# Optimization experiments

Measured on AMD Instinct MI355X. Metric: run time of the kernel, lower is better.

The kernel has to match this reference:

```python
import math
import jax, jax.numpy as jnp
import numpy as np

jax.config.update("jax_enable_x64", True)

# ---- module hyperparameters (init_kwargs) ----
BS, NDIM, NSTEP, ORDER = 16, 16, 128, 2
NIV, NIVSTEPS = 2, 1
P = ORDER + 1                 # number of derivative channels u^(0)..u^(order)
N = NSTEP * P                 # unknowns per system
FACT = np.array([math.factorial(k) for k in range(P)], dtype=np.float64)

# Hard initial-value constraint matrix C (same sparsity for every system)
_C = np.zeros((NIVSTEPS * NIV, N), dtype=np.float64)
for _t in range(NIVSTEPS):
    for _i in range(NIV):
        _C[_t * NIV + _i, _t * P + _i] = 1.0
C = jnp.asarray(_C)
NC = C.shape[0]


def setup_inputs() -> dict:
    key = jax.random.key(0)
    k1, k2, k3, k4 = jax.random.split(key, 4)
    coeffs = jax.random.normal(k1, (BS, NDIM, NSTEP, P), dtype=jnp.float32)
    rhs = jax.random.normal(k2, (BS, NDIM, NSTEP), dtype=jnp.float32)
    iv_rhs = jax.random.normal(k3, (BS, NDIM, NIVSTEPS, NIV), dtype=jnp.float32)
    # step sizes must be positive; keep them in [0.1, 0.2] for good conditioning
    steps = 0.1 + 0.1 * jax.random.uniform(k4, (BS, NDIM, NSTEP - 1), dtype=jnp.float32)
    return {"coeffs": coeffs, "rhs": rhs, "iv_rhs": iv_rhs, "steps": steps}


def _build_A(coeffs, h):
    """Soft-constraint matrix for one scalar ODE system.
    coeffs: (NSTEP, P) f64   ODE coefficients per step
    h:      (NSTEP-1,) f64   step sizes
    Rows: [equation | fwd/bwd Taylor smoothness per order | top-order diff].
    Smoothness rows are normalized by the local truncation error h^(order+1-i).
    """
    n = NSTEP
    t = jnp.arange(n - 1)
    # equation constraints: sum_i c[t,i] u[t,i] = rhs[t]
    A_eq = jnp.zeros((n, N)).at[jnp.repeat(jnp.arange(n), P), jnp.arange(N)].set(coeffs.ravel())
    blocks = [A_eq]
    for i in range(ORDER):
        scale = h ** (-(ORDER + 1 - i))          # (n-1,)
        Af = jnp.zeros((n - 1, N))
        Ab = jnp.zeros((n - 1, N))
        for j in range(i, P):
            cf = (h ** (j - i)) / FACT[j - i]
            cb = ((-h) ** (j - i)) / FACT[j - i]
            Af = Af.at[t, t * P + j].set(scale * cf)        # forward Taylor from step t
            Ab = Ab.at[t, (t + 1) * P + j].set(scale * cb)  # backward Taylor from step t+1
        Af = Af.at[t, (t + 1) * P + i].set(-scale)
        Ab = Ab.at[t, t * P + i].set(-scale)
        blocks += [Af, Ab]
    # highest derivative varies slowly: (u[t+1,K] - u[t,K]) / h ~ 0
    Atop = (jnp.zeros((n - 1, N))
            .at[t, (t + 1) * P + ORDER].set(1.0 / h)
            .at[t, t * P + ORDER].set(-1.0 / h))
    blocks.append(Atop)
    return jnp.concatenate(blocks, axis=0)   # (m, N), m = n + 2(n-1)K + (n-1)


def _solve_one(coeffs, rhs, iv, h):
    """min ||A u - b||^2  s.t.  C u = iv  (KKT solve), one system."""
    A = _build_A(coeffs, h)
    m = A.shape[0]
    b = jnp.concatenate([rhs, jnp.zeros(m - NSTEP)])
    G = A.T @ A                                  # (N, N) banded normal matrix
    Atb = A.T @ b
    M = jnp.block([[G, C.T], [C, jnp.zeros((NC, NC))]])
    v = jnp.concatenate([Atb, iv.ravel()])
    x = jnp.linalg.solve(M, v)
    return x[:N].reshape(NSTEP, P)


def reference(coeffs, rhs, iv_rhs, steps):
    coeffs64 = coeffs.reshape(BS, NDIM, NSTEP, P).astype(jnp.float64)
    rhs64 = rhs.reshape(BS, NDIM, NSTEP).astype(jnp.float64)
    iv64 = iv_rhs.reshape(BS, NDIM, NIVSTEPS, NIV).astype(jnp.float64)
    h64 = steps.reshape(BS, NDIM, NSTEP - 1).astype(jnp.float64)
    solve = jax.vmap(jax.vmap(_solve_one))
    u = solve(coeffs64, rhs64, iv64, h64)        # (BS, NDIM, NSTEP, P)
    u0, u1, u2 = u[..., 0], u[..., 1], u[..., 2]
    return (u0, u1, u2, jnp.zeros(()), h64.reshape(BS * NDIM, NSTEP - 1, 1))
```

## Files before the change

### kernel.cpp

```cpp
#include <hip/hip_runtime.h>
#include <math.h>

#define NSTEP_ 128
#define NSYS_  256
#define STRIDE 21

__device__ __forceinline__ void sym_inv3(const double D[9], double Dinv[9]) {
    const double a = D[0], b = D[3], c = D[4], d = D[6], e = D[7], f = D[8];
    const double A00 = c*f - e*e;
    const double A01 = d*e - b*f;
    const double A02 = b*e - c*d;
    const double A11 = a*f - d*d;
    const double A12 = b*d - a*e;
    const double A22 = a*c - b*b;
    const double det  = a*A00 + b*A01 + d*A02;
    const double idet = 1.0 / det;
    Dinv[0] = A00*idet; Dinv[1] = A01*idet; Dinv[2] = A02*idet;
    Dinv[3] = A01*idet; Dinv[4] = A11*idet; Dinv[5] = A12*idet;
    Dinv[6] = A02*idet; Dinv[7] = A12*idet; Dinv[8] = A22*idet;
}

__device__ __forceinline__ void iface_rows(double h, double wL[5][3], double wR[5][3]) {
    const double ih = 1.0 / h;
    const double s1 = ih * ih;
    const double s0 = s1 * ih;
    const double hh = 0.5 * ih;
    wL[0][0] =  s0; wL[0][1] =  s1; wL[0][2] =  hh;
    wR[0][0] = -s0; wR[0][1] = 0.0; wR[0][2] = 0.0;
    wL[1][0] = -s0; wL[1][1] = 0.0; wL[1][2] = 0.0;
    wR[1][0] =  s0; wR[1][1] = -s1; wR[1][2] =  hh;
    wL[2][0] = 0.0; wL[2][1] =  s1; wL[2][2] =  ih;
    wR[2][0] = 0.0; wR[2][1] = -s1; wR[2][2] = 0.0;
    wL[3][0] = 0.0; wL[3][1] = -s1; wL[3][2] = 0.0;
    wR[3][0] = 0.0; wR[3][1] =  s1; wR[3][2] = -ih;
    wL[4][0] = 0.0; wL[4][1] = 0.0; wL[4][2] = -ih;
    wR[4][0] = 0.0; wR[4][1] = 0.0; wR[4][2] =  ih;
}

__global__ __launch_bounds__(128)
void ode_pcr_solve(const float* __restrict__ coeffs,
                   const float* __restrict__ rhs,
                   const float* __restrict__ ivr,
                   const float* __restrict__ steps,
                   float* __restrict__ out)
{
    const int sys = blockIdx.x;
    const int t   = threadIdx.x;

    const float* cP  = coeffs + (size_t)sys * NSTEP_ * 3;
    const float* rP  = rhs    + (size_t)sys * NSTEP_;
    const float* ivP = ivr    + (size_t)sys * 2;
    const float* hP  = steps  + (size_t)sys * (NSTEP_ - 1);

    __shared__ double sh[NSTEP_ * STRIDE];

    double D[9], U[9], r[3];
    {
        const double cv0 = (double)cP[t*3+0];
        const double cv1 = (double)cP[t*3+1];
        const double cv2 = (double)cP[t*3+2];
        const double rv  = (double)rP[t];
        const double cv[3] = {cv0, cv1, cv2};
        #pragma unroll
        for (int a = 0; a < 3; ++a) {
            #pragma unroll
            for (int b = 0; b < 3; ++b) { D[a*3+b] = cv[a]*cv[b]; U[a*3+b] = 0.0; }
            r[a] = cv[a]*rv;
        }
        if (t < NSTEP_-1) {
            double wL[5][3], wR[5][3];
            iface_rows((double)hP[t], wL, wR);
            #pragma unroll
            for (int k = 0; k < 5; ++k)
                #pragma unroll
                for (int a = 0; a < 3; ++a)
                    #pragma unroll
                    for (int b = 0; b < 3; ++b) {
                        D[a*3+b] += wL[k][a]*wL[k][b];
                        U[a*3+b] += wL[k][a]*wR[k][b];
                    }
        }
        if (t >= 1) {
            double wL[5][3], wR[5][3];
            iface_rows((double)hP[t-1], wL, wR);
            #pragma unroll
            for (int k = 0; k < 5; ++k)
                #pragma unroll
                for (int a = 0; a < 3; ++a)
                    #pragma unroll
                    for (int b = 0; b < 3; ++b)
                        D[a*3+b] += wR[k][a]*wR[k][b];
            if (t == 1) {
                const double iv0 = (double)ivP[0];
                const double iv1 = (double)ivP[1];
                #pragma unroll
                for (int b = 0; b < 3; ++b) {
                    double u0b = 0.0, u1b = 0.0;
                    #pragma unroll
                    for (int k = 0; k < 5; ++k) {
                        u0b += wL[k][0]*wR[k][b];
                        u1b += wL[k][1]*wR[k][b];
                    }
                    r[b] -= u0b*iv0 + u1b*iv1;
                }
            }
        }
        if (t == 0) {
            const double iv0 = (double)ivP[0];
            const double iv1 = (double)ivP[1];
            r[2] -= D[2*3+0]*iv0 + D[2*3+1]*iv1;
            r[0] = iv0; r[1] = iv1;
            #pragma unroll
            for (int a = 0; a < 3; ++a) { D[0*3+a]=0.0; D[1*3+a]=0.0; D[a*3+0]=0.0; D[a*3+1]=0.0; }
            D[0] = 1.0; D[4] = 1.0;
            #pragma unroll
            for (int b = 0; b < 3; ++b) { U[0*3+b] = 0.0; U[1*3+b] = 0.0; }
        }
    }

    #pragma unroll 1
    for (int d = 1; d < NSTEP_; d <<= 1) {
        double Dinv[9];
        sym_inv3(D, Dinv);
        double* row = &sh[t * STRIDE];
        #pragma unroll
        for (int i = 0; i < 9; ++i) row[i]      = Dinv[i];
        #pragma unroll
        for (int i = 0; i < 9; ++i) row[9 + i]  = U[i];
        #pragma unroll
        for (int i = 0; i < 3; ++i) row[18 + i] = r[i];
        __syncthreads();

        double nD[9], nU[9], nr[3];
        #pragma unroll
        for (int i = 0; i < 9; ++i) { nD[i] = D[i]; nU[i] = 0.0; }
        #pragma unroll
        for (int i = 0; i < 3; ++i) nr[i] = r[i];

        if (t + d < NSTEP_) {
            const double* rp_ = &sh[(t + d) * STRIDE];
            double Tp[9];
            #pragma unroll
            for (int a = 0; a < 3; ++a)
                #pragma unroll
                for (int l = 0; l < 3; ++l) {
                    double s = 0.0;
                    #pragma unroll
                    for (int k = 0; k < 3; ++k) s += U[a*3+k] * rp_[k*3+l];
                    Tp[a*3+l] = s;
                }
            #pragma unroll
            for (int a = 0; a < 3; ++a) {
                #pragma unroll
                for (int b = 0; b < 3; ++b) {
                    double su = 0.0, sd = 0.0;
                    #pragma unroll
                    for (int l = 0; l < 3; ++l) {
                        su += Tp[a*3+l] * rp_[9 + l*3+b];
                        sd += Tp[a*3+l] * U[b*3+l];
                    }
                    nU[a*3+b] = -su;
                    nD[a*3+b] -= sd;
                }
                double sr = 0.0;
                #pragma unroll
                for (int l = 0; l < 3; ++l) sr += Tp[a*3+l] * rp_[18 + l];
                nr[a] -= sr;
            }
        }
        if (t - d >= 0) {
            const double* rm_ = &sh[(t - d) * STRIDE];
            double Tm[9];
            #pragma unroll
            for (int a = 0; a < 3; ++a)
                #pragma unroll
                for (int l = 0; l < 3; ++l) {
                    double s = 0.0;
                    #pragma unroll
                    for (int k = 0; k < 3; ++k) s += rm_[9 + k*3+a] * rm_[k*3+l];
                    Tm[a*3+l] = s;
                }
            #pragma unroll
            for (int a = 0; a < 3; ++a) {
                #pragma unroll
                for (int b = 0; b < 3; ++b) {
                    double sd = 0.0;
                    #pragma unroll
                    for (int l = 0; l < 3; ++l) sd += Tm[a*3+l] * rm_[9 + l*3+b];
                    nD[a*3+b] -= sd;
                }
                double sr = 0.0;
                #pragma unroll
                for (int l = 0; l < 3; ++l) sr += Tm[a*3+l] * rm_[18 + l];
                nr[a] -= sr;
            }
        }
        __syncthreads();
        #pragma unroll
        for (int i = 0; i < 9; ++i) { D[i] = nD[i]; U[i] = nU[i]; }
        #pragma unroll
        for (int i = 0; i < 3; ++i) r[i] = nr[i];
    }

    double Dinv[9];
    sym_inv3(D, Dinv);
    const double x0 = Dinv[0]*r[0] + Dinv[1]*r[1] + Dinv[2]*r[2];
    const double x1 = Dinv[3]*r[0] + Dinv[4]*r[1] + Dinv[5]*r[2];
    const double x2 = Dinv[6]*r[0] + Dinv[7]*r[1] + Dinv[8]*r[2];

    float* u0 = out;
    float* u1 = out + 32768;
    float* u2 = out + 65536;
    u0[sys*NSTEP_ + t] = (float)x0;
    u1[sys*NSTEP_ + t] = (float)x1;
    u2[sys*NSTEP_ + t] = (float)x2;

    if (t < NSTEP_-1) out[98305 + sys*(NSTEP_-1) + t] = hP[t];
    if (sys == 0 && t == 0) out[98304] = 0.0f;
}

extern "C" void kernel_launch(void* const* d_in, const int* in_sizes, int n_in,
                              void* d_out, int out_size, void* d_ws, size_t ws_size,
                              hipStream_t stream) {
    const float* coeffs = (const float*)d_in[0];
    const float* rhs    = (const float*)d_in[1];
    const float* ivr    = (const float*)d_in[2];
    const float* steps  = (const float*)d_in[3];
    float* out = (float*)d_out;
    (void)in_sizes; (void)n_in; (void)out_size; (void)d_ws; (void)ws_size;
    hipLaunchKernelGGL(ode_pcr_solve, dim3(NSYS_), dim3(NSTEP_), 0, stream,
                       coeffs, rhs, ivr, steps, out);
}
```

Baseline: 12.63 us.

## Eliminate odd blocks first and run PCR on 64 even blocks in one wavefront

Each thread now owns two consecutive block rows. The odd block is eliminated locally by a Schur complement, which halves the system, and cyclic reduction then runs over 64 even blocks in a single 64-thread wavefront. That cuts the reduction to 6 levels and removes cross-wave barrier cost. The odd unknowns are recovered by back-substitution from their even neighbours. Shared memory becomes a double-buffered structure-of-arrays layout that stores only the symmetric part of Dinv, and outputs are written as float2. The trade-off is more per-thread register pressure in double precision and fewer threads per block, so latency hiding may drop.

Result: faster. 12.05 us (-4.5%).

```diff
diff --git a/kernel.cpp b/kernel.cpp
--- a/kernel.cpp
+++ b/kernel.cpp
@@ -1,9 +1,6 @@
 #include <hip/hip_runtime.h>
-#include <math.h>
-
-#define NSTEP_ 128
-#define NSYS_  256
-#define STRIDE 21
+
+#define NSYS_ 256
 
 __device__ __forceinline__ void sym_inv3(const double D[9], double Dinv[9]) {
     const double a = D[0], b = D[3], c = D[4], d = D[6], e = D[7], f = D[8];
@@ -25,198 +22,257 @@
     const double s1 = ih * ih;
     const double s0 = s1 * ih;
     const double hh = 0.5 * ih;
-    wL[0][0] =  s0; wL[0][1] =  s1; wL[0][2] =  hh;
-    wR[0][0] = -s0; wR[0][1] = 0.0; wR[0][2] = 0.0;
-    wL[1][0] = -s0; wL[1][1] = 0.0; wL[1][2] = 0.0;
-    wR[1][0] =  s0; wR[1][1] = -s1; wR[1][2] =  hh;
-    wL[2][0] = 0.0; wL[2][1] =  s1; wL[2][2] =  ih;
-    wR[2][0] = 0.0; wR[2][1] = -s1; wR[2][2] = 0.0;
-    wL[3][0] = 0.0; wL[3][1] = -s1; wL[3][2] = 0.0;
-    wR[3][0] = 0.0; wR[3][1] =  s1; wR[3][2] = -ih;
-    wL[4][0] = 0.0; wL[4][1] = 0.0; wL[4][2] = -ih;
-    wR[4][0] = 0.0; wR[4][1] = 0.0; wR[4][2] =  ih;
-}
-
-__global__ __launch_bounds__(128)
-void ode_pcr_solve(const float* __restrict__ coeffs,
+    wL[0][0]= s0; wL[0][1]= s1; wL[0][2]= hh;  wR[0][0]=-s0; wR[0][1]=0.0; wR[0][2]=0.0;
+    wL[1][0]=-s0; wL[1][1]=0.0; wL[1][2]=0.0;  wR[1][0]= s0; wR[1][1]=-s1; wR[1][2]= hh;
+    wL[2][0]=0.0; wL[2][1]= s1; wL[2][2]= ih;  wR[2][0]=0.0; wR[2][1]=-s1; wR[2][2]=0.0;
+    wL[3][0]=0.0; wL[3][1]=-s1; wL[3][2]=0.0;  wR[3][0]=0.0; wR[3][1]= s1; wR[3][2]=-ih;
+    wL[4][0]=0.0; wL[4][1]=0.0; wL[4][2]=-ih;  wR[4][0]=0.0; wR[4][1]=0.0; wR[4][2]= ih;
+}
+
+__global__ __launch_bounds__(64)
+void ode_pcr_1wave(const float* __restrict__ coeffs,
                    const float* __restrict__ rhs,
                    const float* __restrict__ ivr,
                    const float* __restrict__ steps,
                    float* __restrict__ out)
 {
     const int sys = blockIdx.x;
-    const int t   = threadIdx.x;
-
-    const float* cP  = coeffs + (size_t)sys * NSTEP_ * 3;
-    const float* rP  = rhs    + (size_t)sys * NSTEP_;
+    const int l   = threadIdx.x;
+    const int m0  = 2*l, m1 = 2*l+1;
+
+    const float* cP  = coeffs + (size_t)sys * 384;
+    const float* rP  = rhs    + (size_t)sys * 128;
     const float* ivP = ivr    + (size_t)sys * 2;
-    const float* hP  = steps  + (size_t)sys * (NSTEP_ - 1);
-
-    __shared__ double sh[NSTEP_ * STRIDE];
-
+    const float* hP  = steps  + (size_t)sys * 127;
+
+    __shared__ double ex[2][18][64];
+
+    const float hf0 = hP[m0];
+    const float hf1 = (l < 63) ? hP[m1] : 0.0f;
+
+    double D0[9], U0[9], r0[3], D1[9], U1[9], r1[3];
+    {
+        const double c0[3] = {(double)cP[m0*3+0], (double)cP[m0*3+1], (double)cP[m0*3+2]};
+        const double c1[3] = {(double)cP[m1*3+0], (double)cP[m1*3+1], (double)cP[m1*3+2]};
+        const double rv0 = (double)rP[m0], rv1 = (double)rP[m1];
+        #pragma unroll
+        for (int a=0;a<3;++a){
+          #pragma unroll
+          for (int b=0;b<3;++b){ D0[a*3+b]=c0[a]*c0[b]; D1[a*3+b]=c1[a]*c1[b];
+                                 U0[a*3+b]=0.0;        U1[a*3+b]=0.0; }
+          r0[a]=c0[a]*rv0; r1[a]=c1[a]*rv1;
+        }
+    }
+    {
+        double wL[5][3], wR[5][3];
+        iface_rows((double)hf0, wL, wR);
+        #pragma unroll
+        for (int k=0;k<5;++k)
+          #pragma unroll
+          for (int a=0;a<3;++a)
+            #pragma unroll
+            for (int b=0;b<3;++b){
+              D0[a*3+b] += wL[k][a]*wL[k][b];
+              U0[a*3+b] += wL[k][a]*wR[k][b];
+              D1[a*3+b] += wR[k][a]*wR[k][b];
+            }
+    }
+    if (l >= 1) {
+        double wL[5][3], wR[5][3];
+        iface_rows((double)hP[m0-1], wL, wR);
+        #pragma unroll
+        for (int k=0;k<5;++k)
+          #pragma unroll
+          for (int a=0;a<3;++a)
+            #pragma unroll
+            for (int b=0;b<3;++b)
+              D0[a*3+b] += wR[k][a]*wR[k][b];
+    }
+    if (l < 63) {
+        double wL[5][3], wR[5][3];
+        iface_rows((double)hf1, wL, wR);
+        #pragma unroll
+        for (int k=0;k<5;++k)
+          #pragma unroll
+          for (int a=0;a<3;++a)
+            #pragma unroll
+            for (int b=0;b<3;++b){
+              D1[a*3+b] += wL[k][a]*wL[k][b];
+              U1[a*3+b] += wL[k][a]*wR[k][b];
+            }
+    }
+    if (l == 0) {
+        const double iv0 = (double)ivP[0], iv1 = (double)ivP[1];
+        #pragma unroll
+        for (int b=0;b<3;++b) r1[b] -= U0[0*3+b]*iv0 + U0[1*3+b]*iv1;
+        #pragma unroll
+        for (int b=0;b<3;++b){ U0[0*3+b]=0.0; U0[1*3+b]=0.0; }
+        r0[2] -= D0[6]*iv0 + D0[7]*iv1;
+        r0[0] = iv0; r0[1] = iv1;
+        D0[1]=D0[2]=D0[3]=D0[5]=D0[6]=D0[7]=0.0;
+        D0[0]=1.0; D0[4]=1.0;
+    }
+
+    double TA[9], TB[9], z1[3];
+    {
+        double Dinv1[9]; sym_inv3(D1, Dinv1);
+        #pragma unroll
+        for (int a=0;a<3;++a)
+          #pragma unroll
+          for (int k=0;k<3;++k){
+            double s=0.0, s2=0.0;
+            #pragma unroll
+            for (int j=0;j<3;++j){ s  += U0[a*3+j]*Dinv1[j*3+k];
+                                   s2 += Dinv1[a*3+j]*U1[j*3+k]; }
+            TA[a*3+k]=s; TB[a*3+k]=s2;
+          }
+        #pragma unroll
+        for (int j=0;j<3;++j)
+          z1[j] = Dinv1[j*3+0]*r1[0] + Dinv1[j*3+1]*r1[1] + Dinv1[j*3+2]*r1[2];
+    }
     double D[9], U[9], r[3];
-    {
-        const double cv0 = (double)cP[t*3+0];
-        const double cv1 = (double)cP[t*3+1];
-        const double cv2 = (double)cP[t*3+2];
-        const double rv  = (double)rP[t];
-        const double cv[3] = {cv0, cv1, cv2};
-        #pragma unroll
-        for (int a = 0; a < 3; ++a) {
-            #pragma unroll
-            for (int b = 0; b < 3; ++b) { D[a*3+b] = cv[a]*cv[b]; U[a*3+b] = 0.0; }
-            r[a] = cv[a]*rv;
-        }
-        if (t < NSTEP_-1) {
-            double wL[5][3], wR[5][3];
-            iface_rows((double)hP[t], wL, wR);
-            #pragma unroll
-            for (int k = 0; k < 5; ++k)
+    #pragma unroll
+    for (int a=0;a<3;++a){
+      #pragma unroll
+      for (int b=0;b<3;++b){
+        double sd=0.0, su=0.0;
+        #pragma unroll
+        for (int j=0;j<3;++j){ sd += TA[a*3+j]*U0[b*3+j];
+                               su += TA[a*3+j]*U1[j*3+b]; }
+        D[a*3+b] = D0[a*3+b] - sd;
+        U[a*3+b] = -su;
+      }
+      r[a] = r0[a] - (TA[a*3+0]*r1[0] + TA[a*3+1]*r1[1] + TA[a*3+2]*r1[2]);
+    }
+    {
+        double Cn[9], cn[3];
+        #pragma unroll
+        for (int a=0;a<3;++a){
+          #pragma unroll
+          for (int b=0;b<3;++b){
+            double s=0.0;
+            #pragma unroll
+            for (int j=0;j<3;++j) s += U1[j*3+a]*TB[j*3+b];
+            Cn[a*3+b]=s;
+          }
+          cn[a] = U1[0*3+a]*z1[0] + U1[1*3+a]*z1[1] + U1[2*3+a]*z1[2];
+        }
+        ex[0][0][l]=Cn[0]; ex[0][1][l]=Cn[1]; ex[0][2][l]=Cn[2];
+        ex[0][3][l]=Cn[4]; ex[0][4][l]=Cn[5]; ex[0][5][l]=Cn[8];
+        ex[0][6][l]=cn[0]; ex[0][7][l]=cn[1]; ex[0][8][l]=cn[2];
+    }
+    __syncthreads();
+    if (l >= 1) {
+        const int p = l-1;
+        const double C0=ex[0][0][p], C1=ex[0][1][p], C2=ex[0][2][p],
+                     C3=ex[0][3][p], C4=ex[0][4][p], C5=ex[0][5][p];
+        D[0]-=C0; D[1]-=C1; D[2]-=C2;
+        D[3]-=C1; D[4]-=C3; D[5]-=C4;
+        D[6]-=C2; D[7]-=C4; D[8]-=C5;
+        r[0]-=ex[0][6][p]; r[1]-=ex[0][7][p]; r[2]-=ex[0][8][p];
+    }
+    __syncthreads();
+
+    int s = 0;
+    for (int d = 1; d < 64; d <<= 1, ++s) {
+        double Dinv[9]; sym_inv3(D, Dinv);
+        double (*buf)[64] = ex[s & 1];
+        buf[0][l]=Dinv[0]; buf[1][l]=Dinv[1]; buf[2][l]=Dinv[2];
+        buf[3][l]=Dinv[4]; buf[4][l]=Dinv[5]; buf[5][l]=Dinv[8];
+        #pragma unroll
+        for (int i=0;i<9;++i) buf[6+i][l]=U[i];
+        buf[15][l]=r[0]; buf[16][l]=r[1]; buf[17][l]=r[2];
+        __syncthreads();
+
+        double nD[9], nU[9], nr[3];
+        #pragma unroll
+        for (int i=0;i<9;++i){ nD[i]=D[i]; nU[i]=0.0; }
+        nr[0]=r[0]; nr[1]=r[1]; nr[2]=r[2];
+
+        if (l + d < 64) {
+            const int p = l + d;
+            double Dp[9], Up[9], rp[3];
+            Dp[0]=buf[0][p]; Dp[1]=buf[1][p]; Dp[2]=buf[2][p];
+            Dp[3]=Dp[1];     Dp[4]=buf[3][p]; Dp[5]=buf[4][p];
+            Dp[6]=Dp[2];     Dp[7]=Dp[5];     Dp[8]=buf[5][p];
+            #pragma unroll
+            for (int i=0;i<9;++i) Up[i]=buf[6+i][p];
+            rp[0]=buf[15][p]; rp[1]=buf[16][p]; rp[2]=buf[17][p];
+            double Tp[9];
+            #pragma unroll
+            for (int a=0;a<3;++a)
+              #pragma unroll
+              for (int k=0;k<3;++k)
+                Tp[a*3+k] = U[a*3+0]*Dp[0*3+k] + U[a*3+1]*Dp[1*3+k] + U[a*3+2]*Dp[2*3+k];
+            #pragma unroll
+            for (int a=0;a<3;++a){
+              #pragma unroll
+              for (int b=0;b<3;++b){
+                double su=0.0, sd=0.0;
                 #pragma unroll
-                for (int a = 0; a < 3; ++a)
-                    #pragma unroll
-                    for (int b = 0; b < 3; ++b) {
-                        D[a*3+b] += wL[k][a]*wL[k][b];
-                        U[a*3+b] += wL[k][a]*wR[k][b];
-                    }
-        }
-        if (t >= 1) {
-            double wL[5][3], wR[5][3];
-            iface_rows((double)hP[t-1], wL, wR);
-            #pragma unroll
-            for (int k = 0; k < 5; ++k)
+                for (int j=0;j<3;++j){ su += Tp[a*3+j]*Up[j*3+b]; sd += Tp[a*3+j]*U[b*3+j]; }
+                nU[a*3+b] = -su;
+                nD[a*3+b] -= sd;
+              }
+              nr[a] -= Tp[a*3+0]*rp[0] + Tp[a*3+1]*rp[1] + Tp[a*3+2]*rp[2];
+            }
+        }
+        if (l - d >= 0) {
+            const int p = l - d;
+            double Dm[9], Um[9], rm[3];
+            Dm[0]=buf[0][p]; Dm[1]=buf[1][p]; Dm[2]=buf[2][p];
+            Dm[3]=Dm[1];     Dm[4]=buf[3][p]; Dm[5]=buf[4][p];
+            Dm[6]=Dm[2];     Dm[7]=Dm[5];     Dm[8]=buf[5][p];
+            #pragma unroll
+            for (int i=0;i<9;++i) Um[i]=buf[6+i][p];
+            rm[0]=buf[15][p]; rm[1]=buf[16][p]; rm[2]=buf[17][p];
+            double Tm[9];
+            #pragma unroll
+            for (int a=0;a<3;++a)
+              #pragma unroll
+              for (int k=0;k<3;++k)
+                Tm[a*3+k] = Um[0*3+a]*Dm[0*3+k] + Um[1*3+a]*Dm[1*3+k] + Um[2*3+a]*Dm[2*3+k];
+            #pragma unroll
+            for (int a=0;a<3;++a){
+              #pragma unroll
+              for (int b=0;b<3;++b){
+                double sd=0.0;
                 #pragma unroll
-                for (int a = 0; a < 3; ++a)
-                    #pragma unroll
-                    for (int b = 0; b < 3; ++b)
-                        D[a*3+b] += wR[k][a]*wR[k][b];
-            if (t == 1) {
-                const double iv0 = (double)ivP[0];
-                const double iv1 = (double)ivP[1];
-                #pragma unroll
-                for (int b = 0; b < 3; ++b) {
-                    double u0b = 0.0, u1b = 0.0;
-                    #pragma unroll
-                    for (int k = 0; k < 5; ++k) {
-                        u0b += wL[k][0]*wR[k][b];
-                        u1b += wL[k][1]*wR[k][b];
-                    }
-                    r[b] -= u0b*iv0 + u1b*iv1;
-                }
-            }
-        }
-        if (t == 0) {
-            const double iv0 = (double)ivP[0];
-            const double iv1 = (double)ivP[1];
-            r[2] -= D[2*3+0]*iv0 + D[2*3+1]*iv1;
-            r[0] = iv0; r[1] = iv1;
-            #pragma unroll
-            for (int a = 0; a < 3; ++a) { D[0*3+a]=0.0; D[1*3+a]=0.0; D[a*3+0]=0.0; D[a*3+1]=0.0; }
-            D[0] = 1.0; D[4] = 1.0;
-            #pragma unroll
-            for (int b = 0; b < 3; ++b) { U[0*3+b] = 0.0; U[1*3+b] = 0.0; }
-        }
-    }
-
-    #pragma unroll 1
-    for (int d = 1; d < NSTEP_; d <<= 1) {
-        double Dinv[9];
-        sym_inv3(D, Dinv);
-        double* row = &sh[t * STRIDE];
-        #pragma unroll
-        for (int i = 0; i < 9; ++i) row[i]      = Dinv[i];
-        #pragma unroll
-        for (int i = 0; i < 9; ++i) row[9 + i]  = U[i];
-        #pragma unroll
-        for (int i = 0; i < 3; ++i) row[18 + i] = r[i];
-        __syncthreads();
-
-        double nD[9], nU[9], nr[3];
-        #pragma unroll
-        for (int i = 0; i < 9; ++i) { nD[i] = D[i]; nU[i] = 0.0; }
-        #pragma unroll
-        for (int i = 0; i < 3; ++i) nr[i] = r[i];
-
-        if (t + d < NSTEP_) {
-            const double* rp_ = &sh[(t + d) * STRIDE];
-            double Tp[9];
-            #pragma unroll
-            for (int a = 0; a < 3; ++a)
-                #pragma unroll
-                for (int l = 0; l < 3; ++l) {
-                    double s = 0.0;
-                    #pragma unroll
-                    for (int k = 0; k < 3; ++k) s += U[a*3+k] * rp_[k*3+l];
-                    Tp[a*3+l] = s;
-                }
-            #pragma unroll
-            for (int a = 0; a < 3; ++a) {
-                #pragma unroll
-                for (int b = 0; b < 3; ++b) {
-                    double su = 0.0, sd = 0.0;
-                    #pragma unroll
-                    for (int l = 0; l < 3; ++l) {
-                        su += Tp[a*3+l] * rp_[9 + l*3+b];
-                        sd += Tp[a*3+l] * U[b*3+l];
-                    }
-                    nU[a*3+b] = -su;
-                    nD[a*3+b] -= sd;
-                }
-                double sr = 0.0;
-                #pragma unroll
-                for (int l = 0; l < 3; ++l) sr += Tp[a*3+l] * rp_[18 + l];
-                nr[a] -= sr;
-            }
-        }
-        if (t - d >= 0) {
-            const double* rm_ = &sh[(t - d) * STRIDE];
-            double Tm[9];
-            #pragma unroll
-            for (int a = 0; a < 3; ++a)
-                #pragma unroll
-                for (int l = 0; l < 3; ++l) {
-                    double s = 0.0;
-                    #pragma unroll
-                    for (int k = 0; k < 3; ++k) s += rm_[9 + k*3+a] * rm_[k*3+l];
-                    Tm[a*3+l] = s;
-                }
-            #pragma unroll
-            for (int a = 0; a < 3; ++a) {
-                #pragma unroll
-                for (int b = 0; b < 3; ++b) {
-                    double sd = 0.0;
-                    #pragma unroll
-                    for (int l = 0; l < 3; ++l) sd += Tm[a*3+l] * rm_[9 + l*3+b];
-                    nD[a*3+b] -= sd;
-                }
-                double sr = 0.0;
-                #pragma unroll
-                for (int l = 0; l < 3; ++l) sr += Tm[a*3+l] * rm_[18 + l];
-                nr[a] -= sr;
-            }
-        }
-        __syncthreads();
-        #pragma unroll
-        for (int i = 0; i < 9; ++i) { D[i] = nD[i]; U[i] = nU[i]; }
-        #pragma unroll
-        for (int i = 0; i < 3; ++i) r[i] = nr[i];
-    }
-
-    double Dinv[9];
-    sym_inv3(D, Dinv);
-    const double x0 = Dinv[0]*r[0] + Dinv[1]*r[1] + Dinv[2]*r[2];
-    const double x1 = Dinv[3]*r[0] + Dinv[4]*r[1] + Dinv[5]*r[2];
-    const double x2 = Dinv[6]*r[0] + Dinv[7]*r[1] + Dinv[8]*r[2];
-
-    float* u0 = out;
-    float* u1 = out + 32768;
-    float* u2 = out + 65536;
-    u0[sys*NSTEP_ + t] = (float)x0;
-    u1[sys*NSTEP_ + t] = (float)x1;
-    u2[sys*NSTEP_ + t] = (float)x2;
-
-    if (t < NSTEP_-1) out[98305 + sys*(NSTEP_-1) + t] = hP[t];
-    if (sys == 0 && t == 0) out[98304] = 0.0f;
+                for (int j=0;j<3;++j) sd += Tm[a*3+j]*Um[j*3+b];
+                nD[a*3+b] -= sd;
+              }
+              nr[a] -= Tm[a*3+0]*rm[0] + Tm[a*3+1]*rm[1] + Tm[a*3+2]*rm[2];
+            }
+        }
+        #pragma unroll
+        for (int i=0;i<9;++i){ D[i]=nD[i]; U[i]=nU[i]; }
+        r[0]=nr[0]; r[1]=nr[1]; r[2]=nr[2];
+    }
+
+    double Dinv[9]; sym_inv3(D, Dinv);
+    const double xe0 = Dinv[0]*r[0] + Dinv[1]*r[1] + Dinv[2]*r[2];
+    const double xe1 = Dinv[3]*r[0] + Dinv[4]*r[1] + Dinv[5]*r[2];
+    const double xe2 = Dinv[6]*r[0] + Dinv[7]*r[1] + Dinv[8]*r[2];
+    ex[0][0][l]=xe0; ex[0][1][l]=xe1; ex[0][2][l]=xe2;
+    __syncthreads();
+    double xN[3] = {0.0, 0.0, 0.0};
+    if (l < 63) { xN[0]=ex[0][0][l+1]; xN[1]=ex[0][1][l+1]; xN[2]=ex[0][2][l+1]; }
+    double xo[3];
+    #pragma unroll
+    for (int j=0;j<3;++j)
+        xo[j] = z1[j] - (TA[0*3+j]*xe0 + TA[1*3+j]*xe1 + TA[2*3+j]*xe2)
+                      - (TB[j*3+0]*xN[0] + TB[j*3+1]*xN[1] + TB[j*3+2]*xN[2]);
+
+    float2* o0 = (float2*)(out)         + (size_t)sys*64;
+    float2* o1 = (float2*)(out + 32768) + (size_t)sys*64;
+    float2* o2 = (float2*)(out + 65536) + (size_t)sys*64;
+    o0[l] = make_float2((float)xe0, (float)xo[0]);
+    o1[l] = make_float2((float)xe1, (float)xo[1]);
+    o2[l] = make_float2((float)xe2, (float)xo[2]);
+    float* outH = out + 98305 + (size_t)sys*127;
+    outH[m0] = hf0;
+    if (l < 63) outH[m1] = hf1;
+    if (sys == 0 && l == 0) out[98304] = 0.0f;
 }
 
 extern "C" void kernel_launch(void* const* d_in, const int* in_sizes, int n_in,
@@ -228,6 +284,6 @@
     const float* steps  = (const float*)d_in[3];
     float* out = (float*)d_out;
     (void)in_sizes; (void)n_in; (void)out_size; (void)d_ws; (void)ws_size;
-    hipLaunchKernelGGL(ode_pcr_solve, dim3(NSYS_), dim3(NSTEP_), 0, stream,
+    hipLaunchKernelGGL(ode_pcr_1wave, dim3(NSYS_), dim3(64), 0, stream,
                        coeffs, rhs, ivr, steps, out);
 }
```
